# Optimization experiments

Measured on AMD Instinct MI355X. Metric: run time of the kernel, lower is better.

Reference implementation:

```python
import jax, jax.numpy as jnp
import numpy as np

TD_DENOM = 3600.0  # td_upper - td_lower
SD_DENOM = 1000.0  # sd_upper - sd_lower

B, T, E, H = 64, 256, 512, 512
V, NB = 50000, 128


def setup_inputs() -> dict:
    key = jax.random.key(0)
    ks = jax.random.split(key, 16)
    s = 0.02
    return {
        'loc_seq': jax.random.randint(ks[0], (B, T), 0, V),
        'td_upper_seq': jax.random.randint(ks[1], (B, T), 0, NB),
        'td_lower_seq': jax.random.randint(ks[2], (B, T), 0, NB),
        'sd_upper_seq': jax.random.randint(ks[3], (B, T), 0, NB),
        'sd_lower_seq': jax.random.randint(ks[4], (B, T), 0, NB),
        'valid_lengths': jax.random.randint(ks[5], (B,), 1, T + 1),
        'loc_emb': jax.random.normal(ks[6], (V, E), jnp.float32) * s,
        't_up_emb': jax.random.normal(ks[7], (NB, E), jnp.float32) * s,
        't_lo_emb': jax.random.normal(ks[8], (NB, E), jnp.float32) * s,
        's_up_emb': jax.random.normal(ks[9], (NB, E), jnp.float32) * s,
        's_lo_emb': jax.random.normal(ks[10], (NB, E), jnp.float32) * s,
        'Wt': jax.random.normal(ks[11], (E, 3 * H), jnp.float32) * s,
        'Ws': jax.random.normal(ks[12], (E, 3 * H), jnp.float32) * s,
        'Wi': jax.random.normal(ks[13], (E, 4 * H), jnp.float32) * s,
        'bi': jnp.zeros((4 * H,), jnp.float32),
        'Wh': jax.random.normal(ks[14], (H, 4 * H), jnp.float32) * s,
    }


def reference(loc_seq, td_upper_seq, td_lower_seq, sd_upper_seq, sd_lower_seq,
              valid_lengths, loc_emb, t_up_emb, t_lo_emb, s_up_emb, s_lo_emb,
              Wt, Ws, Wi, bi, Wh):
    Bs, Ts = loc_seq.shape
    Hs = Wh.shape[0]
    x = loc_emb[loc_seq]                                            # (B,T,E)
    q = (t_up_emb[td_upper_seq] + t_lo_emb[td_lower_seq]) / TD_DENOM
    sp = (s_up_emb[sd_upper_seq] + s_lo_emb[sd_lower_seq]) / SD_DENOM
    # first_step zeroes q and s
    mask = (jnp.arange(Ts) > 0).astype(x.dtype)[None, :, None]
    q = q * mask
    sp = sp * mask
    Fp = jnp.einsum('bte,ef->btf', q, Wt) + jnp.einsum('bte,ef->btf', sp, Ws)  # (B,T,3H)
    xp = jnp.einsum('bte,ef->btf', x, Wi) + bi                                  # (B,T,4H)

    def step(carry, xs):
        h, c = carry
        xpt, Ft = xs
        tmp = xpt + h @ Wh
        i_t, f_t, o_t, g_t = jnp.split(tmp, 4, axis=1)
        i_F, f_F, o_F = jnp.split(Ft, 3, axis=1)
        i_t = jax.nn.sigmoid(i_t + i_F)
        f_t = jax.nn.sigmoid(f_t + f_F)
        o_t = jax.nn.sigmoid(o_t + o_F)
        g_t = jnp.tanh(g_t)
        c = f_t * c + i_t * g_t
        h = o_t * jnp.tanh(c)
        return (h, c), (h, c)

    h0 = jnp.zeros((Bs, Hs), x.dtype)
    c0 = jnp.zeros((Bs, Hs), x.dtype)
    (hT, cT), (hs, cs) = jax.lax.scan(
        step, (h0, c0), (xp.transpose(1, 0, 2), Fp.transpose(1, 0, 2)))
    all_h = hs.transpose(1, 0, 2)  # (B,T,H)
    all_c = cs.transpose(1, 0, 2)
    # original prepends the final hidden, then selects index (valid_length+1)-1
    all_h_full = jnp.concatenate([hT[:, None], all_h], axis=1)  # (B,T+1,H)
    all_c_full = jnp.concatenate([cT[:, None], all_c], axis=1)
    b_idx = jnp.arange(Bs)
    last_h = all_h_full[b_idx, valid_lengths]
    last_c = all_c_full[b_idx, valid_lengths]
    return (all_h, last_h, last_c)
```

## Files before the change

### kernel.cpp

```cpp
#include <hip/hip_runtime.h>
#include <stdint.h>

#define A_CAT_OFF  0ull
#define WCT_OFF    50331648ull
#define WHR_OFF    56623104ull
#define G_OFF      58720256ull
#define HBUF_OFF   125829120ull
#define SENT_OFF   126091264ull
#define WS_NEED    126091520ull

typedef short bf16x8 __attribute__((ext_vector_type(8)));
typedef float f32x4  __attribute__((ext_vector_type(4)));

__device__ __forceinline__ unsigned short f2bf(float f) {
  union { float f; uint32_t u; } v; v.f = f;
  uint32_t u = v.u;
  u += 0x7FFFu + ((u >> 16) & 1u);
  return (unsigned short)(u >> 16);
}
__device__ __forceinline__ float bf2f(unsigned short h) {
  union { uint32_t u; float f; } v; v.u = ((uint32_t)h) << 16;
  return v.f;
}
__device__ __forceinline__ float u2f(uint32_t u) {
  union { uint32_t u; float f; } v; v.u = u; return v.f;
}
__device__ __forceinline__ uint32_t f2u(float f) {
  union { float f; uint32_t u; } v; v.f = f; return v.u;
}
__device__ __forceinline__ float fsigmoid(float x) { return 1.0f / (1.0f + __expf(-x)); }
__device__ __forceinline__ float ftanh(float x) {
  float e = __expf(2.0f * x);
  return 1.0f - 2.0f / (e + 1.0f);
}
__device__ __forceinline__ uint4 pack8(const unsigned short* v) {
  uint4 r;
  r.x = (uint32_t)v[0] | ((uint32_t)v[1] << 16);
  r.y = (uint32_t)v[2] | ((uint32_t)v[3] << 16);
  r.z = (uint32_t)v[4] | ((uint32_t)v[5] << 16);
  r.w = (uint32_t)v[6] | ((uint32_t)v[7] << 16);
  return r;
}

#define GLOAD_LDS16(GP, LP)                                                   \
  __builtin_amdgcn_global_load_lds(                                          \
      (const __attribute__((address_space(1))) uint32_t*)(GP),               \
      (__attribute__((address_space(3))) uint32_t*)(LP), 16, 0, 0)

__global__ __launch_bounds__(256) void k_prep(
    const float* __restrict__ Wi, const float* __restrict__ Wt,
    const float* __restrict__ Ws, const float* __restrict__ Wh,
    uint8_t* ws) {
  int id = blockIdx.x * 256 + threadIdx.x;
  if (id < 393216) {
    int n  = id & 2047;
    int k0 = (id >> 11) << 3;
    unsigned short v[8];
#pragma unroll
    for (int j = 0; j < 8; ++j) {
      int k = k0 + j;
      float x;
      if (k < 512)       x = Wi[k * 2048 + n];
      else if (k < 1024) x = (n < 1536) ? Wt[(k - 512) * 1536 + n] : 0.0f;
      else               x = (n < 1536) ? Ws[(k - 1024) * 1536 + n] : 0.0f;
      v[j] = f2bf(x);
    }
    size_t off = WCT_OFF + (size_t)n * 3072 +
                 (size_t)(((uint32_t)k0 * 2u) ^ (((uint32_t)n & 7u) << 4));
    *(uint4*)(ws + off) = pack8(v);
  } else if (id < 524288) {
    int id2 = id - 393216;
    int cc  = id2 & 2047;
    int k0  = (id2 >> 11) << 3;
    int col = ((cc >> 5) & 3) * 512 + (cc >> 7) * 32 + (cc & 31);
    unsigned short v[8];
#pragma unroll
    for (int j = 0; j < 8; ++j) v[j] = f2bf(Wh[(size_t)(k0 + j) * 2048 + col]);
    *(uint4*)(ws + WHR_OFF + (size_t)cc * 1024 + (size_t)k0 * 2) = pack8(v);
  } else if (id < 532480) {
    uint4 z; z.x = z.y = z.z = z.w = 0u;
    *(uint4*)(ws + HBUF_OFF + (size_t)(id - 524288) * 16) = z;
  } else if (id < 532496) {
    uint4 z; z.x = z.y = z.z = z.w = 0u;
    *(uint4*)(ws + SENT_OFF + (size_t)(id - 532480) * 16) = z;
  }
}

__global__ __launch_bounds__(192) void k_gather(
    const int* __restrict__ loc, const int* __restrict__ tdu,
    const int* __restrict__ tdl, const int* __restrict__ sdu,
    const int* __restrict__ sdl,
    const float* __restrict__ loc_emb, const float* __restrict__ tup,
    const float* __restrict__ tlo, const float* __restrict__ sup,
    const float* __restrict__ slo, uint8_t* ws) {
  int m  = blockIdx.x;
  int t  = m & 255;
  int k0 = threadIdx.x << 3;
  float vals[8];
  if (k0 < 512) {
    const float* s = loc_emb + (size_t)loc[m] * 512 + k0;
#pragma unroll
    for (int j = 0; j < 8; ++j) vals[j] = s[j];
  } else if (k0 < 1024) {
    int e = k0 - 512;
    const float* a = tup + (size_t)tdu[m] * 512 + e;
    const float* b = tlo + (size_t)tdl[m] * 512 + e;
    float sc = (t > 0) ? (1.0f / 3600.0f) : 0.0f;
#pragma unroll
    for (int j = 0; j < 8; ++j) vals[j] = (a[j] + b[j]) * sc;
  } else {
    int e = k0 - 1024;
    const float* a = sup + (size_t)sdu[m] * 512 + e;
    const float* b = slo + (size_t)sdl[m] * 512 + e;
    float sc = (t > 0) ? (1.0f / 1000.0f) : 0.0f;
#pragma unroll
    for (int j = 0; j < 8; ++j) vals[j] = (a[j] + b[j]) * sc;
  }
  unsigned short v[8];
#pragma unroll
  for (int j = 0; j < 8; ++j) v[j] = f2bf(vals[j]);
  size_t off = A_CAT_OFF + (size_t)m * 3072 +
               (size_t)(((uint32_t)k0 * 2u) ^ (((uint32_t)m & 7u) << 4));
  *(uint4*)(ws + off) = pack8(v);
}

__global__ __launch_bounds__(256) void k_gemm(uint8_t* ws,
                                              const float* __restrict__ bi) {
  __shared__ uint8_t A_lds[16384];
  __shared__ uint8_t B_lds[16384];
  const uint8_t* Acat = ws + A_CAT_OFF;
  const uint8_t* Wct  = ws + WCT_OFF;
  uint8_t* Gp = ws + G_OFF;
  int tid = threadIdx.x;
  int lane = tid & 63, wave = tid >> 6;
  int wm = wave >> 1, wn = wave & 1;
  int tile_m = blockIdx.x >> 4, tile_n = blockIdx.x & 15;

  f32x4 acc[4][4];
#pragma unroll
  for (int m = 0; m < 4; ++m)
#pragma unroll
    for (int n = 0; n < 4; ++n) acc[m][n] = f32x4{0.f, 0.f, 0.f, 0.f};

  for (int kb = 0; kb < 1536; kb += 64) {
#pragma unroll
    for (int i = 0; i < 4; ++i) {
      int lidx = i * 256 + tid;
      int row = lidx >> 3, ch = lidx & 7;
      GLOAD_LDS16(Acat + (size_t)(tile_m * 128 + row) * 3072 + kb * 2 + ch * 16,
                  A_lds + (i * 256 + wave * 64) * 16);
    }
#pragma unroll
    for (int i = 0; i < 4; ++i) {
      int lidx = i * 256 + tid;
      int row = lidx >> 3, ch = lidx & 7;
      GLOAD_LDS16(Wct + (size_t)(tile_n * 128 + row) * 3072 + kb * 2 + ch * 16,
                  B_lds + (i * 256 + wave * 64) * 16);
    }
    __syncthreads();
#pragma unroll
    for (int kk = 0; kk < 2; ++kk) {
      int koff = kk * 64 + ((lane >> 4) << 4);
      bf16x8 af[4], bfr[4];
#pragma unroll
      for (int m = 0; m < 4; ++m) {
        int row = wm * 64 + m * 16 + (lane & 15);
        af[m] = *(const bf16x8*)(A_lds + row * 128 + (koff ^ ((row & 7) << 4)));
      }
#pragma unroll
      for (int n = 0; n < 4; ++n) {
        int row = wn * 64 + n * 16 + (lane & 15);
        bfr[n] = *(const bf16x8*)(B_lds + row * 128 + (koff ^ ((row & 7) << 4)));
      }
#pragma unroll
      for (int m = 0; m < 4; ++m)
#pragma unroll
        for (int n = 0; n < 4; ++n)
          acc[m][n] = __builtin_amdgcn_mfma_f32_16x16x32_bf16(af[m], bfr[n],
                                                              acc[m][n], 0, 0, 0);
    }
    __syncthreads();
  }
  int lr = lane >> 4, lc = lane & 15;
#pragma unroll
  for (int n = 0; n < 4; ++n) {
    int gcol = tile_n * 128 + wn * 64 + n * 16 + lc;
    float bv = bi[gcol];
#pragma unroll
    for (int m = 0; m < 4; ++m) {
      int growb = tile_m * 128 + wm * 64 + m * 16 + lr * 4;
#pragma unroll
      for (int q = 0; q < 4; ++q) {
        int grow = growb + q;
        float v = acc[m][n][q] + bv;
        size_t gi = ((size_t)(grow & 255) * 64 + (size_t)(grow >> 8)) * 2048 + gcol;
        *(unsigned short*)(Gp + gi * 2) = f2bf(v);
      }
    }
  }
}

__global__ __launch_bounds__(512, 2) void k_recur(uint8_t* ws,
                                                  const int* __restrict__ vlen,
                                                  float* __restrict__ out) {
  int bid = blockIdx.x;
  if ((bid & 7) >= 4) return;
  int r = bid & 7, c = bid >> 3;

  extern __shared__ uint8_t smem[];
  uint8_t* h_lds = smem;
  float*   tmp   = (float*)(smem + 16384);

  int tid = threadIdx.x;
  int lane = tid & 63, wave = tid >> 6;

  const uint8_t* Gp  = ws + G_OFF;
  const uint8_t* Whr = ws + WHR_OFF;
  uint32_t* sent = (uint32_t*)(ws + SENT_OFF) + r * 16;

  bf16x8 Bfrag[16];
  {
    int cc = c * 128 + wave * 16 + (lane & 15);
    const uint8_t* wb = Whr + (size_t)cc * 1024 + ((lane >> 4) << 4);
#pragma unroll
    for (int kk = 0; kk < 16; ++kk)
      Bfrag[kk] = *(const bf16x8*)(wb + kk * 64);
  }

  int gb = tid >> 5, d = tid & 31;
  int gbatch = r * 16 + gb;
  int vl = vlen[gbatch];
  float cr = 0.0f, hprev = 0.0f, cprev = 0.0f;
  bool fb = false;

  int hb_b = 2 * wave + (lane >> 5);
  int hb_byte = (lane & 31) * 64;

  float* outH  = out;
  float* outLH = out + 8388608;
  float* outLC = out + 8421376;

  __syncthreads();

  for (int t = 0; t < 256; ++t) {
    {
      const uint32_t* sp = sent + (lane & 15);
      int passes = 0;
      for (;;) {
        uint32_t sv;
        if (!fb) {
          asm volatile("global_load_dword %0, %1, off sc0\n\t"
                       "s_waitcnt vmcnt(0)"
                       : "=v"(sv) : "v"(sp) : "memory");
          __builtin_amdgcn_sched_barrier(0);
        } else {
          sv = __hip_atomic_load(sp, __ATOMIC_RELAXED, __HIP_MEMORY_SCOPE_AGENT);
        }
        if (__ballot(sv >= (uint32_t)t) == ~0ULL) break;
        if (++passes > 64) fb = true;
      }
    }
    uint64_t x[8];
    {
      const uint8_t* hb = ws + HBUF_OFF + (size_t)(t & 1) * 131072 +
                          (size_t)(r * 16 + hb_b) * 2048 + hb_byte;
      if (!fb) {
#pragma unroll
        for (int i = 0; i < 8; ++i) {
          const void* p = hb + i * 8;
          asm volatile("global_load_dwordx2 %0, %1, off sc0"
                       : "=v"(x[i]) : "v"(p) : "memory");
        }
        asm volatile("s_waitcnt vmcnt(0)" ::: "memory");
        __builtin_amdgcn_sched_barrier(0);
      } else {
#pragma unroll
        for (int i = 0; i < 8; ++i)
          x[i] = __hip_atomic_load((const uint64_t*)(hb + i * 8),
                                   __ATOMIC_RELAXED, __HIP_MEMORY_SCOPE_AGENT);
      }
    }
    unsigned short gv0, gv1, gv2, gv3;
    {
      const uint8_t* gp = Gp + (size_t)(t * 64 + gbatch) * 4096 +
                          (size_t)(c * 64 + d * 2);
      gv0 = *(const unsigned short*)(gp);
      gv1 = *(const unsigned short*)(gp + 1024);
      gv2 = *(const unsigned short*)(gp + 2048);
      gv3 = *(const unsigned short*)(gp + 3072);
    }
    if (t > 0) {
      outH[((size_t)gbatch * 256 + (size_t)(t - 1)) * 512 + (size_t)(c * 32 + d)] = hprev;
      if (t - 1 == vl - 1) {
        size_t lb = (size_t)gbatch * 512 + (size_t)(c * 32 + d);
        outLH[lb] = hprev;
        outLC[lb] = cprev;
      }
    }
    {
      uint32_t w[8];
#pragma unroll
      for (int i = 0; i < 8; ++i) {
        uint32_t lo = (uint32_t)x[i], hi = (uint32_t)(x[i] >> 32);
        w[i] = (uint32_t)f2bf(u2f(lo)) | ((uint32_t)f2bf(u2f(hi)) << 16);
      }
      int base = hb_b * 1024 + (lane & 31) * 32;
      int swz = (hb_b & 7) << 4;
      uint4 v0; v0.x = w[0]; v0.y = w[1]; v0.z = w[2]; v0.w = w[3];
      uint4 v1; v1.x = w[4]; v1.y = w[5]; v1.z = w[6]; v1.w = w[7];
      *(uint4*)(h_lds + (base ^ swz)) = v0;
      *(uint4*)(h_lds + ((base + 16) ^ swz)) = v1;
    }
    __syncthreads();

    f32x4 acc = f32x4{0.f, 0.f, 0.f, 0.f};
    {
      int lrow = lane & 15;
      int g16 = (lane >> 4) << 4;
      int aswz = (lrow & 7) << 4;
#pragma unroll
      for (int kk = 0; kk < 16; ++kk) {
        bf16x8 a = *(const bf16x8*)(h_lds + lrow * 1024 + ((kk * 64 + g16) ^ aswz));
        acc = __builtin_amdgcn_mfma_f32_16x16x32_bf16(a, Bfrag[kk], acc, 0, 0, 0);
      }
    }
    {
      int colb = wave * 16 + (lane & 15);
      int rowd = (lane >> 4) << 2;
#pragma unroll
      for (int q = 0; q < 4; ++q)
        tmp[(rowd + q) * 132 + colb] = acc[q];
    }
    __syncthreads();

    float hval, cval;
    {
      int tb = gb * 132 + d;
      float ip = tmp[tb]      + bf2f(gv0);
      float fp = tmp[tb + 32] + bf2f(gv1);
      float op = tmp[tb + 64] + bf2f(gv2);
      float gp = tmp[tb + 96] + bf2f(gv3);
      float ig = fsigmoid(ip), fg = fsigmoid(fp), og = fsigmoid(op);
      float gt = ftanh(gp);
      cval = fg * cr + ig * gt;
      cr = cval;
      hval = og * ftanh(cval);
    }
    {
      uint32_t hw = f2u(hval);
      uint32_t* pub = (uint32_t*)(ws + HBUF_OFF + (size_t)((t + 1) & 1) * 131072 +
                                  (size_t)gbatch * 2048 + (size_t)(c * 32 + d) * 4);
      asm volatile("global_store_dword %0, %1, off" :: "v"(pub), "v"(hw) : "memory");
      __hip_atomic_store(pub, hw, __ATOMIC_RELAXED, __HIP_MEMORY_SCOPE_AGENT);
    }
    hprev = hval; cprev = cval;
    asm volatile("s_waitcnt vmcnt(0)" ::: "memory");
    __syncthreads();
    if (tid == 0) {
      uint32_t sval = (uint32_t)(t + 1);
      uint32_t* sc = sent + c;
      asm volatile("global_store_dword %0, %1, off" :: "v"(sc), "v"(sval) : "memory");
      __hip_atomic_store(sc, sval, __ATOMIC_RELAXED, __HIP_MEMORY_SCOPE_AGENT);
    }
  }
  outH[((size_t)gbatch * 256 + 255) * 512 + (size_t)(c * 32 + d)] = hprev;
  if (vl == 256) {
    size_t lb = (size_t)gbatch * 512 + (size_t)(c * 32 + d);
    outLH[lb] = hprev;
    outLC[lb] = cprev;
  }
}

extern "C" void kernel_launch(void* const* d_in, const int* in_sizes, int n_in,
                              void* d_out, int out_size, void* d_ws, size_t ws_size,
                              hipStream_t stream) {
  const int*   loc     = (const int*)d_in[0];
  const int*   tdu     = (const int*)d_in[1];
  const int*   tdl     = (const int*)d_in[2];
  const int*   sdu     = (const int*)d_in[3];
  const int*   sdl     = (const int*)d_in[4];
  const int*   vlen    = (const int*)d_in[5];
  const float* loc_emb = (const float*)d_in[6];
  const float* tup     = (const float*)d_in[7];
  const float* tlo     = (const float*)d_in[8];
  const float* sup     = (const float*)d_in[9];
  const float* slo     = (const float*)d_in[10];
  const float* Wt      = (const float*)d_in[11];
  const float* Ws      = (const float*)d_in[12];
  const float* Wi      = (const float*)d_in[13];
  const float* bi      = (const float*)d_in[14];
  const float* Wh      = (const float*)d_in[15];
  uint8_t* ws = (uint8_t*)d_ws;
  float* out = (float*)d_out;

  if (ws_size < WS_NEED) return;

  (void)hipFuncSetAttribute((const void*)k_recur,
                            hipFuncAttributeMaxDynamicSharedMemorySize, 98304);

  k_prep  <<<2081, 256, 0, stream>>>(Wi, Wt, Ws, Wh, ws);
  k_gather<<<16384, 192, 0, stream>>>(loc, tdu, tdl, sdu, sdl,
                                      loc_emb, tup, tlo, sup, slo, ws);
  k_gemm  <<<2048, 256, 0, stream>>>(ws, bi);
  k_recur <<<128, 512, 98304, stream>>>(ws, vlen, out);
}
```

Measured before the change: 1.297 ms.

## Replace sentinel flags with parity-tagged hidden-state words for cross-block sync

Removes the separate per-column sentinel array and the end-of-step vmcnt wait plus block barrier. Instead, each published h value carries a step-parity tag in its low mantissa bit, and consumers spin on the h buffer itself until every word shows the expected tag. It also prefetches the next step's gate inputs, splits the MFMA accumulation into two chains, and uses lighter LDS-only barriers. This cuts one global round trip and one barrier per step. In exchange, h loses its lowest mantissa bit, which is negligible since h is rounded to bf16 anyway, and the fallback path adds a republish store.

```diff
diff --git a/kernel.cpp b/kernel.cpp
--- a/kernel.cpp
+++ b/kernel.cpp
@@ -6,8 +6,7 @@
 #define WHR_OFF    56623104ull
 #define G_OFF      58720256ull
 #define HBUF_OFF   125829120ull
-#define SENT_OFF   126091264ull
-#define WS_NEED    126091520ull
+#define WS_NEED    126091264ull
 
 typedef short bf16x8 __attribute__((ext_vector_type(8)));
 typedef float f32x4  __attribute__((ext_vector_type(4)));
@@ -46,6 +45,13 @@
   __builtin_amdgcn_global_load_lds(                                          \
       (const __attribute__((address_space(1))) uint32_t*)(GP),               \
       (__attribute__((address_space(3))) uint32_t*)(LP), 16, 0, 0)
+
+#define BAR_LDS()                                                             \
+  do {                                                                        \
+    asm volatile("s_waitcnt lgkmcnt(0)" ::: "memory");                        \
+    __builtin_amdgcn_sched_barrier(0);                                        \
+    __builtin_amdgcn_s_barrier();                                             \
+  } while (0)
 
 __global__ __launch_bounds__(256) void k_prep(
     const float* __restrict__ Wi, const float* __restrict__ Wt,
@@ -80,9 +86,9 @@
   } else if (id < 532480) {
     uint4 z; z.x = z.y = z.z = z.w = 0u;
     *(uint4*)(ws + HBUF_OFF + (size_t)(id - 524288) * 16) = z;
-  } else if (id < 532496) {
-    uint4 z; z.x = z.y = z.z = z.w = 0u;
-    *(uint4*)(ws + SENT_OFF + (size_t)(id - 532480) * 16) = z;
+  } else if (id < 540672) {
+    uint4 z; z.x = z.y = z.z = z.w = 1u;
+    *(uint4*)(ws + HBUF_OFF + 131072ull + (size_t)(id - 532480) * 16) = z;
   }
 }
 
@@ -216,7 +222,6 @@
 
   const uint8_t* Gp  = ws + G_OFF;
   const uint8_t* Whr = ws + WHR_OFF;
-  uint32_t* sent = (uint32_t*)(ws + SENT_OFF) + r * 16;
 
   bf16x8 Bfrag[16];
   {
@@ -231,6 +236,7 @@
   int gbatch = r * 16 + gb;
   int vl = vlen[gbatch];
   float cr = 0.0f, hprev = 0.0f, cprev = 0.0f;
+  uint32_t pubw_prev = 0;
   bool fb = false;
 
   int hb_b = 2 * wave + (lane >> 5);
@@ -240,61 +246,54 @@
   float* outLH = out + 8388608;
   float* outLC = out + 8421376;
 
+  const uint8_t* gthr = Gp + ((size_t)gbatch * 4096 + (size_t)(c * 64 + d * 2));
+  unsigned short gc0 = *(const unsigned short*)(gthr);
+  unsigned short gc1 = *(const unsigned short*)(gthr + 1024);
+  unsigned short gc2 = *(const unsigned short*)(gthr + 2048);
+  unsigned short gc3 = *(const unsigned short*)(gthr + 3072);
+
   __syncthreads();
 
   for (int t = 0; t < 256; ++t) {
-    {
-      const uint32_t* sp = sent + (lane & 15);
+    uint64_t x[8];
+    {
+      const uint8_t* hb = ws + HBUF_OFF + (size_t)(t & 1) * 131072 +
+                          (size_t)(r * 16 + hb_b) * 2048 + hb_byte;
+      uint32_t expect = (uint32_t)((t >> 1) & 1);
       int passes = 0;
       for (;;) {
-        uint32_t sv;
         if (!fb) {
-          asm volatile("global_load_dword %0, %1, off sc0\n\t"
-                       "s_waitcnt vmcnt(0)"
-                       : "=v"(sv) : "v"(sp) : "memory");
+#pragma unroll
+          for (int i = 0; i < 8; ++i) {
+            const void* p = hb + i * 8;
+            asm volatile("global_load_dwordx2 %0, %1, off sc0"
+                         : "=v"(x[i]) : "v"(p) : "memory");
+          }
+          asm volatile("s_waitcnt vmcnt(0)" ::: "memory");
           __builtin_amdgcn_sched_barrier(0);
         } else {
-          sv = __hip_atomic_load(sp, __ATOMIC_RELAXED, __HIP_MEMORY_SCOPE_AGENT);
+#pragma unroll
+          for (int i = 0; i < 8; ++i)
+            x[i] = __hip_atomic_load((const uint64_t*)(hb + i * 8),
+                                     __ATOMIC_RELAXED, __HIP_MEMORY_SCOPE_AGENT);
         }
-        if (__ballot(sv >= (uint32_t)t) == ~0ULL) break;
-        if (++passes > 64) fb = true;
-      }
-    }
-    uint64_t x[8];
-    {
-      const uint8_t* hb = ws + HBUF_OFF + (size_t)(t & 1) * 131072 +
-                          (size_t)(r * 16 + hb_b) * 2048 + hb_byte;
-      if (!fb) {
+        uint32_t bad = 0;
 #pragma unroll
         for (int i = 0; i < 8; ++i) {
-          const void* p = hb + i * 8;
-          asm volatile("global_load_dwordx2 %0, %1, off sc0"
-                       : "=v"(x[i]) : "v"(p) : "memory");
+          uint32_t lo = (uint32_t)x[i], hi = (uint32_t)(x[i] >> 32);
+          bad |= ((lo ^ expect) & 1u) | ((hi ^ expect) & 1u);
         }
-        asm volatile("s_waitcnt vmcnt(0)" ::: "memory");
-        __builtin_amdgcn_sched_barrier(0);
-      } else {
-#pragma unroll
-        for (int i = 0; i < 8; ++i)
-          x[i] = __hip_atomic_load((const uint64_t*)(hb + i * 8),
-                                   __ATOMIC_RELAXED, __HIP_MEMORY_SCOPE_AGENT);
-      }
-    }
-    unsigned short gv0, gv1, gv2, gv3;
-    {
-      const uint8_t* gp = Gp + (size_t)(t * 64 + gbatch) * 4096 +
-                          (size_t)(c * 64 + d * 2);
-      gv0 = *(const unsigned short*)(gp);
-      gv1 = *(const unsigned short*)(gp + 1024);
-      gv2 = *(const unsigned short*)(gp + 2048);
-      gv3 = *(const unsigned short*)(gp + 3072);
-    }
-    if (t > 0) {
-      outH[((size_t)gbatch * 256 + (size_t)(t - 1)) * 512 + (size_t)(c * 32 + d)] = hprev;
-      if (t - 1 == vl - 1) {
-        size_t lb = (size_t)gbatch * 512 + (size_t)(c * 32 + d);
-        outLH[lb] = hprev;
-        outLC[lb] = cprev;
+        if (!bad) break;
+        if (++passes > 256 && !fb) {
+          fb = true;
+          if (t > 0) {
+            uint32_t* pp = (uint32_t*)(ws + HBUF_OFF + (size_t)(t & 1) * 131072 +
+                                       (size_t)gbatch * 2048 +
+                                       (size_t)(c * 32 + d) * 4);
+            __hip_atomic_store(pp, pubw_prev, __ATOMIC_RELAXED,
+                               __HIP_MEMORY_SCOPE_AGENT);
+          }
+        }
       }
     }
     {
@@ -311,17 +310,42 @@
       *(uint4*)(h_lds + (base ^ swz)) = v0;
       *(uint4*)(h_lds + ((base + 16) ^ swz)) = v1;
     }
-    __syncthreads();
-
-    f32x4 acc = f32x4{0.f, 0.f, 0.f, 0.f};
+    BAR_LDS();
+
+    if (t > 0) {
+      if (!fb) {
+        uint32_t* pp = (uint32_t*)(ws + HBUF_OFF + (size_t)(t & 1) * 131072 +
+                                   (size_t)gbatch * 2048 + (size_t)(c * 32 + d) * 4);
+        __hip_atomic_store(pp, pubw_prev, __ATOMIC_RELAXED,
+                           __HIP_MEMORY_SCOPE_AGENT);
+      }
+      outH[((size_t)gbatch * 256 + (size_t)(t - 1)) * 512 + (size_t)(c * 32 + d)] = hprev;
+      if (t - 1 == vl - 1) {
+        size_t lb = (size_t)gbatch * 512 + (size_t)(c * 32 + d);
+        outLH[lb] = hprev;
+        outLC[lb] = cprev;
+      }
+    }
+    unsigned short gn0, gn1, gn2, gn3;
+    {
+      const uint8_t* gp = gthr + (size_t)((t + 1) & 255) * 262144;
+      gn0 = *(const unsigned short*)(gp);
+      gn1 = *(const unsigned short*)(gp + 1024);
+      gn2 = *(const unsigned short*)(gp + 2048);
+      gn3 = *(const unsigned short*)(gp + 3072);
+    }
+
+    f32x4 acc0 = f32x4{0.f, 0.f, 0.f, 0.f}, acc1 = acc0;
     {
       int lrow = lane & 15;
       int g16 = (lane >> 4) << 4;
       int aswz = (lrow & 7) << 4;
 #pragma unroll
-      for (int kk = 0; kk < 16; ++kk) {
-        bf16x8 a = *(const bf16x8*)(h_lds + lrow * 1024 + ((kk * 64 + g16) ^ aswz));
-        acc = __builtin_amdgcn_mfma_f32_16x16x32_bf16(a, Bfrag[kk], acc, 0, 0, 0);
+      for (int kk = 0; kk < 16; kk += 2) {
+        bf16x8 a0 = *(const bf16x8*)(h_lds + lrow * 1024 + ((kk * 64 + g16) ^ aswz));
+        bf16x8 a1 = *(const bf16x8*)(h_lds + lrow * 1024 + (((kk + 1) * 64 + g16) ^ aswz));
+        acc0 = __builtin_amdgcn_mfma_f32_16x16x32_bf16(a0, Bfrag[kk], acc0, 0, 0, 0);
+        acc1 = __builtin_amdgcn_mfma_f32_16x16x32_bf16(a1, Bfrag[kk + 1], acc1, 0, 0, 0);
       }
     }
     {
@@ -329,17 +353,17 @@
       int rowd = (lane >> 4) << 2;
 #pragma unroll
       for (int q = 0; q < 4; ++q)
-        tmp[(rowd + q) * 132 + colb] = acc[q];
-    }
-    __syncthreads();
+        tmp[(rowd + q) * 132 + colb] = acc0[q] + acc1[q];
+    }
+    BAR_LDS();
 
     float hval, cval;
     {
       int tb = gb * 132 + d;
-      float ip = tmp[tb]      + bf2f(gv0);
-      float fp = tmp[tb + 32] + bf2f(gv1);
-      float op = tmp[tb + 64] + bf2f(gv2);
-      float gp = tmp[tb + 96] + bf2f(gv3);
+      float ip = tmp[tb]      + bf2f(gc0);
+      float fp = tmp[tb + 32] + bf2f(gc1);
+      float op = tmp[tb + 64] + bf2f(gc2);
+      float gp = tmp[tb + 96] + bf2f(gc3);
       float ig = fsigmoid(ip), fg = fsigmoid(fp), og = fsigmoid(op);
       float gt = ftanh(gp);
       cval = fg * cr + ig * gt;
@@ -347,21 +371,17 @@
       hval = og * ftanh(cval);
     }
     {
-      uint32_t hw = f2u(hval);
+      uint32_t wtag = (uint32_t)(((t + 1) >> 1) & 1);
+      uint32_t pubw = (f2u(hval) & ~1u) | wtag;
       uint32_t* pub = (uint32_t*)(ws + HBUF_OFF + (size_t)((t + 1) & 1) * 131072 +
                                   (size_t)gbatch * 2048 + (size_t)(c * 32 + d) * 4);
-      asm volatile("global_store_dword %0, %1, off" :: "v"(pub), "v"(hw) : "memory");
-      __hip_atomic_store(pub, hw, __ATOMIC_RELAXED, __HIP_MEMORY_SCOPE_AGENT);
+      asm volatile("global_store_dword %0, %1, off" :: "v"(pub), "v"(pubw) : "memory");
+      if (fb)
+        __hip_atomic_store(pub, pubw, __ATOMIC_RELAXED, __HIP_MEMORY_SCOPE_AGENT);
+      pubw_prev = pubw;
     }
     hprev = hval; cprev = cval;
-    asm volatile("s_waitcnt vmcnt(0)" ::: "memory");
-    __syncthreads();
-    if (tid == 0) {
-      uint32_t sval = (uint32_t)(t + 1);
-      uint32_t* sc = sent + c;
-      asm volatile("global_store_dword %0, %1, off" :: "v"(sc), "v"(sval) : "memory");
-      __hip_atomic_store(sc, sval, __ATOMIC_RELAXED, __HIP_MEMORY_SCOPE_AGENT);
-    }
+    gc0 = gn0; gc1 = gn1; gc2 = gn2; gc3 = gn3;
   }
   outH[((size_t)gbatch * 256 + 255) * 512 + (size_t)(c * 32 + d)] = hprev;
   if (vl == 256) {
@@ -398,7 +418,7 @@
   (void)hipFuncSetAttribute((const void*)k_recur,
                             hipFuncAttributeMaxDynamicSharedMemorySize, 98304);
 
-  k_prep  <<<2081, 256, 0, stream>>>(Wi, Wt, Ws, Wh, ws);
+  k_prep  <<<2112, 256, 0, stream>>>(Wi, Wt, Ws, Wh, ws);
   k_gather<<<16384, 192, 0, stream>>>(loc, tdu, tdl, sdu, sdl,
                                       loc_emb, tup, tlo, sup, slo, ws);
   k_gemm  <<<2048, 256, 0, stream>>>(ws, bi);
```

Result: slower. 2.014 ms (+55.3%).
